# Kernel tuning notes

Measured on AMD Instinct MI355X. Metric: run time of the kernel, lower is better.

## Reference

```python
import jax, jax.numpy as jnp
import numpy as np

K, N, GROUP = 4096, 12288, 64
M = 4096  # tokens (batch*seq)


def setup_inputs() -> dict:
    key = jax.random.key(0)
    k1, k2, k3, k4, k5 = jax.random.split(key, 5)
    input = jax.random.normal(k1, (M, K), dtype=jnp.float32)
    qweight = jax.random.randint(k2, (K, N), 0, 4, dtype=jnp.int32)  # int2 codes in [0,4)
    scale = jax.random.uniform(k3, (K // GROUP, N), dtype=jnp.float32)
    zp = jax.random.normal(k4, (K // GROUP, N), dtype=jnp.float32)
    bias = jax.random.normal(k5, (N,), dtype=jnp.float32)
    return {"input": input, "qweight": qweight, "scale": scale, "zp": zp, "bias": bias}


def reference(input, qweight, scale, zp, bias):
    # Group-wise asymmetric dequant: W[k,n] = q[k,n]*scale[k//g,n] + zp[k//g,n]
    G = K // GROUP
    q = qweight.astype(input.dtype).reshape(G, GROUP, N)
    w = q * scale[:, None, :] + zp[:, None, :]          # [G, g, N]
    w = w.reshape(K, N)
    out = input @ w + bias[None, :]                      # [M, N]
    return out
```

## Files before the change

kernel.cpp:

```cpp
#include <hip/hip_runtime.h>
#include <hip/hip_bf16.h>

#define Mdim 4096
#define Kdim 4096
#define Ndim 12288

typedef __attribute__((ext_vector_type(8))) short short8;
typedef __attribute__((ext_vector_type(4))) float floatx4;
typedef __attribute__((ext_vector_type(4))) int intx4;
typedef __attribute__((ext_vector_type(4))) unsigned short ushortx4;
typedef __attribute__((ext_vector_type(8))) unsigned short ushortx8;

static __device__ __forceinline__ unsigned short f2bf(float x) {
    __hip_bfloat16 h = __float2bfloat16(x);
    return __builtin_bit_cast(unsigned short, h);
}

static __device__ __forceinline__ void gload_lds16(const unsigned short* g, unsigned short* l) {
    __builtin_amdgcn_global_load_lds(
        (const __attribute__((address_space(1))) unsigned int*)g,
        (__attribute__((address_space(3))) unsigned int*)l,
        16, 0, 0);
}

#define DQ_BLOCKS 3072
#define XC_BLOCKS 2048

__global__ void __launch_bounds__(256)
prep(const int* __restrict__ Q, const float* __restrict__ S,
     const float* __restrict__ Z, unsigned short* __restrict__ Wt,
     const float* __restrict__ X, unsigned short* __restrict__ Xw)
{
    const int t = threadIdx.x;
    if (blockIdx.x < DQ_BLOCKS) {
        __shared__ unsigned short Ls[4][64][72];
        const int b     = blockIdx.x;
        const int kbase = (b & 15) * 256;
        const int n0    = (b >> 4) * 64;
        const int tn = t & 15, tk = t >> 4;
        const int nc = tn * 4;

        floatx4 s4[4], z4[4];
        intx4 q[4][4];
        #pragma unroll
        for (int s = 0; s < 4; ++s) {
            const int k0 = kbase + s * 64;
            const int g  = k0 >> 6;
            s4[s] = *reinterpret_cast<const floatx4*>(&S[(size_t)g * Ndim + n0 + nc]);
            z4[s] = *reinterpret_cast<const floatx4*>(&Z[(size_t)g * Ndim + n0 + nc]);
            #pragma unroll
            for (int r = 0; r < 4; ++r)
                q[s][r] = *reinterpret_cast<const intx4*>(
                    &Q[(size_t)(k0 + tk * 4 + r) * Ndim + n0 + nc]);
        }
        #pragma unroll
        for (int s = 0; s < 4; ++s) {
            #pragma unroll
            for (int j = 0; j < 4; ++j) {
                const float sv = s4[s][j], zv = z4[s][j];
                ushortx4 w;
                w.x = f2bf(fmaf((float)q[s][0][j], sv, zv));
                w.y = f2bf(fmaf((float)q[s][1][j], sv, zv));
                w.z = f2bf(fmaf((float)q[s][2][j], sv, zv));
                w.w = f2bf(fmaf((float)q[s][3][j], sv, zv));
                *reinterpret_cast<ushortx4*>(&Ls[s][nc + j][tk * 4]) = w;
            }
        }
        __syncthreads();
        const int n_o = t >> 5;
        const int ko  = (t & 31) * 8;
        const int so  = ko >> 6;
        const int kc  = ko & 63;
        #pragma unroll
        for (int p = 0; p < 8; ++p) {
            const int n = n_o + p * 8;
            const ushortx8 v = *reinterpret_cast<const ushortx8*>(&Ls[so][n][kc]);
            *reinterpret_cast<ushortx8*>(
                &Wt[(size_t)(n0 + n) * Kdim + kbase + ko]) = v;
        }
    } else {
        const int xb = blockIdx.x - DQ_BLOCKS;
        const size_t stride = (size_t)XC_BLOCKS * 256 * 8;
        size_t base = ((size_t)xb * 256 + t) * 8;
        floatx4 a[4], b2[4];
        #pragma unroll
        for (int it = 0; it < 4; ++it) {
            a[it]  = *reinterpret_cast<const floatx4*>(&X[base + it * stride]);
            b2[it] = *reinterpret_cast<const floatx4*>(&X[base + it * stride + 4]);
        }
        #pragma unroll
        for (int it = 0; it < 4; ++it) {
            ushortx8 w;
            w[0] = f2bf(a[it].x); w[1] = f2bf(a[it].y);
            w[2] = f2bf(a[it].z); w[3] = f2bf(a[it].w);
            w[4] = f2bf(b2[it].x); w[5] = f2bf(b2[it].y);
            w[6] = f2bf(b2[it].z); w[7] = f2bf(b2[it].w);
            *reinterpret_cast<ushortx8*>(&Xw[base + it * stride]) = w;
        }
    }
}


#define STAGE_A(c, kt, h) do { \
    const unsigned short* sp_ = A + aoff + (size_t)((h) * 128) * Kdim + (size_t)(kt) * 64; \
    unsigned short* dp_ = &As[c][((h) * 128 + wave * 16) * 64]; \
    gload_lds16(sp_, dp_); \
    gload_lds16(sp_ + (size_t)8 * Kdim, dp_ + 8 * 64); \
} while (0)

#define STAGE_B(c, kt, h) do { \
    const unsigned short* sp_ = B + boff + (size_t)((h) * 128) * Kdim + (size_t)(kt) * 64; \
    unsigned short* dp_ = &Bs[c][((h) * 128 + wave * 16) * 64]; \
    gload_lds16(sp_, dp_); \
    gload_lds16(sp_ + (size_t)8 * Kdim, dp_ + 8 * 64); \
} while (0)

#define LDA_(c, i, kh) (*reinterpret_cast<const short8*>( \
    &As[c][(wm + (i) * 16 + lrow) * 64 + (((kh) * 4 + quad) ^ lsw) * 8]))
#define LDB_(c, j, kh) (*reinterpret_cast<const short8*>( \
    &Bs[c][(wn + (j) * 16 + lrow) * 64 + (((kh) * 4 + quad) ^ lsw) * 8]))

#define SBAR()  __builtin_amdgcn_sched_barrier(0)

#define MFMA_Q(AF, BF, IO, JO) do { \
    __builtin_amdgcn_s_setprio(1); \
    _Pragma("unroll") \
    for (int kh_ = 0; kh_ < 2; ++kh_) { \
        _Pragma("unroll") \
        for (int i_ = 0; i_ < 4; ++i_) { \
            _Pragma("unroll") \
            for (int j_ = 0; j_ < 2; ++j_) { \
                acc[(IO) + i_][(JO) + j_] = __builtin_amdgcn_mfma_f32_16x16x32_bf16( \
                    AF[i_][kh_], BF[j_][kh_], acc[(IO) + i_][(JO) + j_], 0, 0, 0); \
            } \
        } \
    } \
    __builtin_amdgcn_s_setprio(0); \
} while (0)

__global__ void __launch_bounds__(512, 2)
gemm_bf16_8p(const unsigned short* __restrict__ A, const unsigned short* __restrict__ B,
             const float* __restrict__ bias, float* __restrict__ O)
{
    __shared__ unsigned short As[2][256 * 64];
    __shared__ unsigned short Bs[2][256 * 64];

    constexpr int NT = Kdim / 64;

    const int nblk = Ndim / 256;
    const int cpx  = (Mdim / 256) * nblk / 8;
    const int bid  = blockIdx.x;
    const int swz  = (bid & 7) * cpx + (bid >> 3);
    const int gsz  = 8 * nblk;
    const int grp  = swz / gsz;
    const int r    = swz % gsz;
    const int m0   = (grp * 8 + (r & 7)) * 256;
    const int n0   = (r >> 3) * 256;

    const int t    = threadIdx.x;
    const int wave = t >> 6;
    const int lane = t & 63;
    const int wm   = (wave >> 2) * 128;
    const int wn   = (wave & 3) * 64;
    const int lrow = lane & 15;
    const int quad = lane >> 4;
    const int lsw  = lrow & 7;

    const int srow = lane >> 3;
    const int scol = ((lane & 7) ^ srow) * 8;
    const size_t aoff = (size_t)(m0 + wave * 16 + srow) * Kdim + scol;
    const size_t boff = (size_t)(n0 + wave * 16 + srow) * Kdim + scol;

    floatx4 acc[8][4];
    #pragma unroll
    for (int i = 0; i < 8; ++i)
        #pragma unroll
        for (int j = 0; j < 4; ++j)
            acc[i][j] = floatx4{0.f, 0.f, 0.f, 0.f};

    short8 afA[4][2];
    short8 afB[4][2];
    short8 bA[2][2];
    short8 bB[2][2];

    STAGE_A(0, 0, 0); STAGE_A(0, 0, 1);
    STAGE_B(0, 0, 0); STAGE_B(0, 0, 1);
    STAGE_B(1, 1, 0); STAGE_B(1, 1, 1);
    STAGE_A(1, 1, 0);
    asm volatile("s_waitcnt vmcnt(2)" ::: "memory");
    __builtin_amdgcn_s_barrier();
    SBAR();
    #pragma unroll
    for (int i = 0; i < 4; ++i) { afA[i][0] = LDA_(0, i, 0); afA[i][1] = LDA_(0, i, 1); }
    #pragma unroll
    for (int j = 0; j < 2; ++j) { bA[j][0] = LDB_(0, j, 0); bA[j][1] = LDB_(0, j, 1); }
    #pragma unroll
    for (int j = 0; j < 2; ++j) { bB[j][0] = LDB_(0, j + 2, 0); bB[j][1] = LDB_(0, j + 2, 1); }
    asm volatile("s_waitcnt lgkmcnt(0)" ::: "memory");
    SBAR();
    __builtin_amdgcn_s_barrier();
    SBAR();

    for (int u = 0; u < NT; ++u) {
        const int c = u & 1, cn = c ^ 1;

        #pragma unroll
        for (int i = 0; i < 4; ++i) { afB[i][0] = LDA_(c, i + 4, 0); afB[i][1] = LDA_(c, i + 4, 1); }
        if (u + 1 < NT) STAGE_A(cn, u + 1, 1);
        if (u + 2 < NT) STAGE_B(c, u + 2, 0);
        MFMA_Q(afA, bA, 0, 0);
        SBAR();
        __builtin_amdgcn_s_barrier();
        SBAR();

        if (u + 2 < NT) STAGE_B(c, u + 2, 1);
        MFMA_Q(afB, bA, 4, 0);
        SBAR();
        if (u < NT - 2) { asm volatile("s_waitcnt vmcnt(4)" ::: "memory"); }
        else            { asm volatile("s_waitcnt vmcnt(0)" ::: "memory"); }
        __builtin_amdgcn_s_barrier();
        SBAR();

        if (u + 1 < NT) {
            #pragma unroll
            for (int j = 0; j < 2; ++j) { bA[j][0] = LDB_(cn, j, 0); bA[j][1] = LDB_(cn, j, 1); }
        }
        MFMA_Q(afA, bB, 0, 2);
        SBAR();
        __builtin_amdgcn_s_barrier();
        SBAR();

        if (u + 1 < NT) {
            #pragma unroll
            for (int i = 0; i < 4; ++i) { afA[i][0] = LDA_(cn, i, 0); afA[i][1] = LDA_(cn, i, 1); }
        }
        if (u + 2 < NT) STAGE_A(c, u + 2, 0);
        MFMA_Q(afB, bB, 4, 2);
        SBAR();
        if (u + 1 < NT) {
            #pragma unroll
            for (int j = 0; j < 2; ++j) { bB[j][0] = LDB_(cn, j + 2, 0); bB[j][1] = LDB_(cn, j + 2, 1); }
        }
        asm volatile("s_waitcnt lgkmcnt(0)" ::: "memory");
        SBAR();
        __builtin_amdgcn_s_barrier();
        SBAR();
    }

    #pragma unroll
    for (int j = 0; j < 4; ++j) {
        const int col = n0 + wn + j * 16 + lrow;
        const float bv = bias[col];
        #pragma unroll
        for (int i = 0; i < 8; ++i) {
            const int rbase = m0 + wm + i * 16 + quad * 4;
            #pragma unroll
            for (int rr = 0; rr < 4; ++rr)
                O[(size_t)(rbase + rr) * Ndim + col] = acc[i][j][rr] + bv;
        }
    }
}

__global__ void __launch_bounds__(256)
w2a16_gemm_fb(const float* __restrict__ X, const int* __restrict__ Q,
              const float* __restrict__ S, const float* __restrict__ Z,
              const float* __restrict__ bias, float* __restrict__ O)
{
    __shared__ unsigned short Asf[128][72];
    __shared__ unsigned short Bsf[128][72];
    const int t  = threadIdx.x;
    const int n0 = blockIdx.x * 128;
    const int m0 = blockIdx.y * 128;
    const int wave = t >> 6, lane = t & 63;
    const int wm = (wave & 1) * 64, wn = (wave >> 1) * 64;
    const int lrow = lane & 15, quad = lane >> 4;
    floatx4 acc[4][4];
    #pragma unroll
    for (int i = 0; i < 4; ++i)
        #pragma unroll
        for (int j = 0; j < 4; ++j) acc[i][j] = floatx4{0.f, 0.f, 0.f, 0.f};
    const int a_row0 = t >> 4, a_c = (t & 15) * 4;
    const int b_n = t & 127, b_k0 = (t >> 7) * 32;
    for (int k0 = 0; k0 < Kdim; k0 += 64) {
        #pragma unroll
        for (int i = 0; i < 8; ++i) {
            const int row = a_row0 + i * 16;
            const floatx4 v = *reinterpret_cast<const floatx4*>(
                &X[(size_t)(m0 + row) * Kdim + k0 + a_c]);
            ushortx4 w;
            w.x = f2bf(v.x); w.y = f2bf(v.y); w.z = f2bf(v.z); w.w = f2bf(v.w);
            *reinterpret_cast<ushortx4*>(&Asf[row][a_c]) = w;
        }
        const int g = k0 >> 6;
        const float s = S[(size_t)g * Ndim + n0 + b_n];
        const float z = Z[(size_t)g * Ndim + n0 + b_n];
        #pragma unroll
        for (int i = 0; i < 8; ++i) {
            const int kk = b_k0 + i * 4;
            const int* qp = &Q[(size_t)(k0 + kk) * Ndim + n0 + b_n];
            ushortx4 w;
            w.x = f2bf(fmaf((float)qp[0],                s, z));
            w.y = f2bf(fmaf((float)qp[(size_t)Ndim],     s, z));
            w.z = f2bf(fmaf((float)qp[(size_t)2 * Ndim], s, z));
            w.w = f2bf(fmaf((float)qp[(size_t)3 * Ndim], s, z));
            *reinterpret_cast<ushortx4*>(&Bsf[b_n][kk]) = w;
        }
        __syncthreads();
        #pragma unroll
        for (int kk = 0; kk < 64; kk += 32) {
            short8 afv[4], bfv[4];
            #pragma unroll
            for (int i = 0; i < 4; ++i)
                afv[i] = *reinterpret_cast<const short8*>(&Asf[wm + i * 16 + lrow][kk + quad * 8]);
            #pragma unroll
            for (int j = 0; j < 4; ++j)
                bfv[j] = *reinterpret_cast<const short8*>(&Bsf[wn + j * 16 + lrow][kk + quad * 8]);
            #pragma unroll
            for (int i = 0; i < 4; ++i)
                #pragma unroll
                for (int j = 0; j < 4; ++j)
                    acc[i][j] = __builtin_amdgcn_mfma_f32_16x16x32_bf16(afv[i], bfv[j], acc[i][j], 0, 0, 0);
        }
        __syncthreads();
    }
    #pragma unroll
    for (int j = 0; j < 4; ++j) {
        const int col = n0 + wn + j * 16 + lrow;
        const float bv = bias[col];
        #pragma unroll
        for (int i = 0; i < 4; ++i) {
            const int rbase = m0 + wm + i * 16 + quad * 4;
            #pragma unroll
            for (int rr = 0; rr < 4; ++rr)
                O[(size_t)(rbase + rr) * Ndim + col] = acc[i][j][rr] + bv;
        }
    }
}

extern "C" void kernel_launch(void* const* d_in, const int* in_sizes, int n_in,
                              void* d_out, int out_size, void* d_ws, size_t ws_size,
                              hipStream_t stream) {
    const float* X  = (const float*)d_in[0];
    const int*   Q  = (const int*)d_in[1];
    const float* S  = (const float*)d_in[2];
    const float* Z  = (const float*)d_in[3];
    const float* Bi = (const float*)d_in[4];
    float* O = (float*)d_out;

    const size_t wt_bytes = (size_t)Kdim * Ndim * 2;
    const size_t xw_bytes = (size_t)Mdim * Kdim * 2;

    if (ws_size >= wt_bytes + xw_bytes) {
        unsigned short* Wt = (unsigned short*)d_ws;
        unsigned short* Xw = (unsigned short*)((char*)d_ws + wt_bytes);

        hipLaunchKernelGGL(prep, dim3(DQ_BLOCKS + XC_BLOCKS), dim3(256), 0, stream,
                           Q, S, Z, Wt, X, Xw);

        const int nblocks = (Mdim / 256) * (Ndim / 256);
        hipLaunchKernelGGL(gemm_bf16_8p, dim3(nblocks), dim3(512), 0, stream, Xw, Wt, Bi, O);
    } else {
        dim3 grid(Ndim / 128, Mdim / 128);
        hipLaunchKernelGGL(w2a16_gemm_fb, grid, dim3(256), 0, stream, X, Q, S, Z, Bi, O);
    }
}
```

Before: 763.8 us.

## Replace LDS-staged pipelined GEMM with direct global-to-register MFMA loads

Removes the shared-memory double-buffered pipeline (global_load_lds staging, swizzled LDS reads, barriers, sched barriers) and instead has each wave load its A and B fragments directly from global memory into registers every 32-wide K step. This drops LDS traffic and block-level synchronization. In exchange there is no cross-wave data reuse through LDS, so global/L2 traffic rises sharply, and memory latency is hidden only by the unroll and occupancy.

```diff
diff --git a/kernel.cpp b/kernel.cpp
--- a/kernel.cpp
+++ b/kernel.cpp
@@ -14,13 +14,6 @@
 static __device__ __forceinline__ unsigned short f2bf(float x) {
     __hip_bfloat16 h = __float2bfloat16(x);
     return __builtin_bit_cast(unsigned short, h);
-}
-
-static __device__ __forceinline__ void gload_lds16(const unsigned short* g, unsigned short* l) {
-    __builtin_amdgcn_global_load_lds(
-        (const __attribute__((address_space(1))) unsigned int*)g,
-        (__attribute__((address_space(3))) unsigned int*)l,
-        16, 0, 0);
 }
 
 #define DQ_BLOCKS 3072
@@ -100,53 +93,10 @@
     }
 }
 
-
-#define STAGE_A(c, kt, h) do { \
-    const unsigned short* sp_ = A + aoff + (size_t)((h) * 128) * Kdim + (size_t)(kt) * 64; \
-    unsigned short* dp_ = &As[c][((h) * 128 + wave * 16) * 64]; \
-    gload_lds16(sp_, dp_); \
-    gload_lds16(sp_ + (size_t)8 * Kdim, dp_ + 8 * 64); \
-} while (0)
-
-#define STAGE_B(c, kt, h) do { \
-    const unsigned short* sp_ = B + boff + (size_t)((h) * 128) * Kdim + (size_t)(kt) * 64; \
-    unsigned short* dp_ = &Bs[c][((h) * 128 + wave * 16) * 64]; \
-    gload_lds16(sp_, dp_); \
-    gload_lds16(sp_ + (size_t)8 * Kdim, dp_ + 8 * 64); \
-} while (0)
-
-#define LDA_(c, i, kh) (*reinterpret_cast<const short8*>( \
-    &As[c][(wm + (i) * 16 + lrow) * 64 + (((kh) * 4 + quad) ^ lsw) * 8]))
-#define LDB_(c, j, kh) (*reinterpret_cast<const short8*>( \
-    &Bs[c][(wn + (j) * 16 + lrow) * 64 + (((kh) * 4 + quad) ^ lsw) * 8]))
-
-#define SBAR()  __builtin_amdgcn_sched_barrier(0)
-
-#define MFMA_Q(AF, BF, IO, JO) do { \
-    __builtin_amdgcn_s_setprio(1); \
-    _Pragma("unroll") \
-    for (int kh_ = 0; kh_ < 2; ++kh_) { \
-        _Pragma("unroll") \
-        for (int i_ = 0; i_ < 4; ++i_) { \
-            _Pragma("unroll") \
-            for (int j_ = 0; j_ < 2; ++j_) { \
-                acc[(IO) + i_][(JO) + j_] = __builtin_amdgcn_mfma_f32_16x16x32_bf16( \
-                    AF[i_][kh_], BF[j_][kh_], acc[(IO) + i_][(JO) + j_], 0, 0, 0); \
-            } \
-        } \
-    } \
-    __builtin_amdgcn_s_setprio(0); \
-} while (0)
-
 __global__ void __launch_bounds__(512, 2)
-gemm_bf16_8p(const unsigned short* __restrict__ A, const unsigned short* __restrict__ B,
-             const float* __restrict__ bias, float* __restrict__ O)
+gemm_nolds(const unsigned short* __restrict__ A, const unsigned short* __restrict__ B,
+           const float* __restrict__ bias, float* __restrict__ O)
 {
-    __shared__ unsigned short As[2][256 * 64];
-    __shared__ unsigned short Bs[2][256 * 64];
-
-    constexpr int NT = Kdim / 64;
-
     const int nblk = Ndim / 256;
     const int cpx  = (Mdim / 256) * nblk / 8;
     const int bid  = blockIdx.x;
@@ -164,12 +114,9 @@
     const int wn   = (wave & 3) * 64;
     const int lrow = lane & 15;
     const int quad = lane >> 4;
-    const int lsw  = lrow & 7;
-
-    const int srow = lane >> 3;
-    const int scol = ((lane & 7) ^ srow) * 8;
-    const size_t aoff = (size_t)(m0 + wave * 16 + srow) * Kdim + scol;
-    const size_t boff = (size_t)(n0 + wave * 16 + srow) * Kdim + scol;
+
+    const unsigned short* Ab = A + (size_t)(m0 + wm + lrow) * Kdim + quad * 8;
+    const unsigned short* Bb = B + (size_t)(n0 + wn + lrow) * Kdim + quad * 8;
 
     floatx4 acc[8][4];
     #pragma unroll
@@ -178,73 +125,21 @@
         for (int j = 0; j < 4; ++j)
             acc[i][j] = floatx4{0.f, 0.f, 0.f, 0.f};
 
-    short8 afA[4][2];
-    short8 afB[4][2];
-    short8 bA[2][2];
-    short8 bB[2][2];
-
-    STAGE_A(0, 0, 0); STAGE_A(0, 0, 1);
-    STAGE_B(0, 0, 0); STAGE_B(0, 0, 1);
-    STAGE_B(1, 1, 0); STAGE_B(1, 1, 1);
-    STAGE_A(1, 1, 0);
-    asm volatile("s_waitcnt vmcnt(2)" ::: "memory");
-    __builtin_amdgcn_s_barrier();
-    SBAR();
-    #pragma unroll
-    for (int i = 0; i < 4; ++i) { afA[i][0] = LDA_(0, i, 0); afA[i][1] = LDA_(0, i, 1); }
-    #pragma unroll
-    for (int j = 0; j < 2; ++j) { bA[j][0] = LDB_(0, j, 0); bA[j][1] = LDB_(0, j, 1); }
-    #pragma unroll
-    for (int j = 0; j < 2; ++j) { bB[j][0] = LDB_(0, j + 2, 0); bB[j][1] = LDB_(0, j + 2, 1); }
-    asm volatile("s_waitcnt lgkmcnt(0)" ::: "memory");
-    SBAR();
-    __builtin_amdgcn_s_barrier();
-    SBAR();
-
-    for (int u = 0; u < NT; ++u) {
-        const int c = u & 1, cn = c ^ 1;
-
-        #pragma unroll
-        for (int i = 0; i < 4; ++i) { afB[i][0] = LDA_(c, i + 4, 0); afB[i][1] = LDA_(c, i + 4, 1); }
-        if (u + 1 < NT) STAGE_A(cn, u + 1, 1);
-        if (u + 2 < NT) STAGE_B(c, u + 2, 0);
-        MFMA_Q(afA, bA, 0, 0);
-        SBAR();
-        __builtin_amdgcn_s_barrier();
-        SBAR();
-
-        if (u + 2 < NT) STAGE_B(c, u + 2, 1);
-        MFMA_Q(afB, bA, 4, 0);
-        SBAR();
-        if (u < NT - 2) { asm volatile("s_waitcnt vmcnt(4)" ::: "memory"); }
-        else            { asm volatile("s_waitcnt vmcnt(0)" ::: "memory"); }
-        __builtin_amdgcn_s_barrier();
-        SBAR();
-
-        if (u + 1 < NT) {
-            #pragma unroll
-            for (int j = 0; j < 2; ++j) { bA[j][0] = LDB_(cn, j, 0); bA[j][1] = LDB_(cn, j, 1); }
-        }
-        MFMA_Q(afA, bB, 0, 2);
-        SBAR();
-        __builtin_amdgcn_s_barrier();
-        SBAR();
-
-        if (u + 1 < NT) {
-            #pragma unroll
-            for (int i = 0; i < 4; ++i) { afA[i][0] = LDA_(cn, i, 0); afA[i][1] = LDA_(cn, i, 1); }
-        }
-        if (u + 2 < NT) STAGE_A(c, u + 2, 0);
-        MFMA_Q(afB, bB, 4, 2);
-        SBAR();
-        if (u + 1 < NT) {
-            #pragma unroll
-            for (int j = 0; j < 2; ++j) { bB[j][0] = LDB_(cn, j + 2, 0); bB[j][1] = LDB_(cn, j + 2, 1); }
-        }
-        asm volatile("s_waitcnt lgkmcnt(0)" ::: "memory");
-        SBAR();
-        __builtin_amdgcn_s_barrier();
-        SBAR();
+    #pragma unroll 2
+    for (int k0 = 0; k0 < Kdim; k0 += 32) {
+        short8 af[8], bf[4];
+        #pragma unroll
+        for (int i = 0; i < 8; ++i)
+            af[i] = *reinterpret_cast<const short8*>(&Ab[(size_t)i * 16 * Kdim + k0]);
+        #pragma unroll
+        for (int j = 0; j < 4; ++j)
+            bf[j] = *reinterpret_cast<const short8*>(&Bb[(size_t)j * 16 * Kdim + k0]);
+        #pragma unroll
+        for (int i = 0; i < 8; ++i)
+            #pragma unroll
+            for (int j = 0; j < 4; ++j)
+                acc[i][j] = __builtin_amdgcn_mfma_f32_16x16x32_bf16(
+                    af[i], bf[j], acc[i][j], 0, 0, 0);
     }
 
     #pragma unroll
@@ -358,7 +253,7 @@
                            Q, S, Z, Wt, X, Xw);
 
         const int nblocks = (Mdim / 256) * (Ndim / 256);
-        hipLaunchKernelGGL(gemm_bf16_8p, dim3(nblocks), dim3(512), 0, stream, Xw, Wt, Bi, O);
+        hipLaunchKernelGGL(gemm_nolds, dim3(nblocks), dim3(512), 0, stream, Xw, Wt, Bi, O);
     } else {
         dim3 grid(Ndim / 128, Mdim / 128);
         hipLaunchKernelGGL(w2a16_gemm_fb, grid, dim3(256), 0, stream, X, Q, S, Z, Bi, O);
```

Result: slower. 1.432 ms (+87.4%).
